# Optimization experiments

Hardware: AMD Instinct MI355X
Metric: run time of the kernel (lower is better)

The kernel has to match this reference:

```python
import jax, jax.numpy as jnp
import numpy as np

B, C, H, W = 4, 256, 64, 64
DQ = C // 8

def setup_inputs() -> dict:
    key = jax.random.key(0)
    ks = jax.random.split(key, 7)
    x = jax.random.normal(ks[0], (B, C, H, W), dtype=jnp.float32)
    # 1x1 convs == per-pixel linear layers: weight [out, in], bias [out]
    Wq = jax.random.normal(ks[1], (DQ, C), dtype=jnp.float32) * (1.0 / np.sqrt(C))
    bq = jax.random.normal(ks[2], (DQ,), dtype=jnp.float32) * 0.01
    Wk = jax.random.normal(ks[3], (DQ, C), dtype=jnp.float32) * (1.0 / np.sqrt(C))
    bk = jax.random.normal(ks[4], (DQ,), dtype=jnp.float32) * 0.01
    Wv = jax.random.normal(ks[5], (C, C), dtype=jnp.float32) * (1.0 / np.sqrt(C))
    bv = jax.random.normal(ks[6], (C,), dtype=jnp.float32) * 0.01
    return {"x": x, "Wq": Wq, "bq": bq, "Wk": Wk, "bk": bk, "Wv": Wv, "bv": bv}

def reference(x, Wq, bq, Wk, bk, Wv, bv):
    b, c, h, w = x.shape
    n = h * w
    xf = x.reshape(b, c, n)                                  # [b,c,n]
    Q = jnp.einsum('dc,bcn->bnd', Wq, xf) + bq               # [b,n,dq]
    K = jnp.einsum('dc,bcn->bdn', Wk, xf) + bk[None, :, None]  # [b,dq,n]
    A = jax.nn.softmax(jnp.einsum('bnd,bdm->bnm', Q, K), axis=-1)  # [b,n,n]
    V = jnp.einsum('oc,bcn->bon', Wv, xf) + bv[None, :, None]      # [b,c,n]
    # torch: bmm(V, A^T) -> out[b,c,i] = sum_j V[b,c,j] * A[b,i,j]
    out = jnp.einsum('bcj,bij->bci', V, A)
    return x + out.reshape(b, c, h, w)
```

## Files before the change

kernel.cpp:

```cpp
#include <hip/hip_runtime.h>
#include <math.h>

#define BB 4
#define CC 256
#define NN 4096
#define DQ 32
#define LOG2E 1.44269504f

typedef _Float16 half8 __attribute__((ext_vector_type(8)));
typedef _Float16 half4 __attribute__((ext_vector_type(4)));
typedef float float4v __attribute__((ext_vector_type(4)));

__global__ __launch_bounds__(64) void prep_kernel(
    const float* __restrict__ Wq, const float* __restrict__ bq,
    const float* __restrict__ Wk, const float* __restrict__ bk,
    const float* __restrict__ Wv, const float* __restrict__ bv,
    _Float16* __restrict__ Wh, float* __restrict__ bh)
{
    int o = blockIdx.x, t = threadIdx.x;
    const float* src; float scale = 1.0f, bias;
    if (o < DQ)            { src = Wq + o * CC;        scale = LOG2E; bias = bq[o] * LOG2E; }
    else if (o < 2 * DQ)   { src = Wk + (o - DQ) * CC;                bias = bk[o - DQ]; }
    else                   { src = Wv + (o - 2 * DQ) * CC;            bias = bv[o - 2 * DQ]; }
    float4 v = *(const float4*)(src + t * 4);
    half4 h = { (_Float16)(v.x * scale), (_Float16)(v.y * scale),
                (_Float16)(v.z * scale), (_Float16)(v.w * scale) };
    *(half4*)(Wh + o * CC + t * 4) = h;
    if (t == 0) bh[o] = bias;
}

__global__ __launch_bounds__(256) void proj_kernel(
    const float* __restrict__ x, const _Float16* __restrict__ Wh,
    const float* __restrict__ bh,
    _Float16* __restrict__ Qt, _Float16* __restrict__ Kt,
    _Float16* __restrict__ Vh)
{
    __shared__ _Float16 xl[32 * 256];
    __shared__ _Float16 os_qk[32 * 72];
    __shared__ _Float16 os_v[256 * 40];

    const int tid = threadIdx.x;
    const int lane = tid & 63, w = tid >> 6;
    const int i16 = lane & 15, q = lane >> 4;
    const int n0 = blockIdx.x * 32, b = blockIdx.y;

    const float* xb = x + (size_t)b * CC * NN + n0;
    #pragma unroll
    for (int u = 0; u < 8; ++u) {
        int idx = u * 256 + tid;
        int c = idx >> 3, n4 = idx & 7;
        float4 v = *(const float4*)(xb + (size_t)c * NN + n4 * 4);
        int chunk = c >> 3, cl = c & 7;
        float vv[4] = {v.x, v.y, v.z, v.w};
        #pragma unroll
        for (int e = 0; e < 4; ++e) {
            int n = n4 * 4 + e;
            xl[n * 256 + ((chunk ^ n) * 8) + cl] = (_Float16)vv[e];
        }
    }

    float4v acc[5][2];
    const int obase = 80 * w;
    #pragma unroll
    for (int ot = 0; ot < 5; ++ot) {
        float4 b4 = *(const float4*)(bh + obase + 16 * ot + 4 * q);
        #pragma unroll
        for (int nt = 0; nt < 2; ++nt)
            acc[ot][nt] = (float4v){b4.x, b4.y, b4.z, b4.w};
    }
    __syncthreads();

    #pragma unroll
    for (int k = 0; k < 8; ++k) {
        half8 af[5], bf[2];
        #pragma unroll
        for (int ot = 0; ot < 5; ++ot)
            af[ot] = *(const half8*)(Wh + (size_t)(obase + 16 * ot + i16) * CC + k * 32 + 8 * q);
        #pragma unroll
        for (int nt = 0; nt < 2; ++nt) {
            int n = 16 * nt + i16;
            bf[nt] = *(const half8*)&xl[n * 256 + (((4 * k + q) ^ n) * 8)];
        }
        #pragma unroll
        for (int ot = 0; ot < 5; ++ot)
            #pragma unroll
            for (int nt = 0; nt < 2; ++nt)
                acc[ot][nt] = __builtin_amdgcn_mfma_f32_16x16x32_f16(af[ot], bf[nt], acc[ot][nt], 0, 0, 0);
    }

    #pragma unroll
    for (int ot = 0; ot < 5; ++ot) {
        int og = obase + 16 * ot;
        #pragma unroll
        for (int nt = 0; nt < 2; ++nt) {
            int n = 16 * nt + i16;
            if (og < 64) {
                half4 hv = { (_Float16)acc[ot][nt][0], (_Float16)acc[ot][nt][1],
                             (_Float16)acc[ot][nt][2], (_Float16)acc[ot][nt][3] };
                *(half4*)&os_qk[n * 72 + og + 4 * q] = hv;
            } else {
                int cb = og - 64 + 4 * q;
                #pragma unroll
                for (int r = 0; r < 4; ++r)
                    os_v[(cb + r) * 40 + n] = (_Float16)acc[ot][nt][r];
            }
        }
    }
    __syncthreads();

    _Float16* Qtb = Qt + (size_t)b * NN * DQ;
    _Float16* Ktb = Kt + (size_t)b * NN * DQ;
    {
        int n = tid >> 3, p = tid & 7;
        half8 hv = *(const half8*)&os_qk[n * 72 + 8 * p];
        if (p < 4) *(half8*)(Qtb + (size_t)(n0 + n) * DQ + 8 * p) = hv;
        else       *(half8*)(Ktb + (size_t)(n0 + n) * DQ + 8 * (p - 4)) = hv;
    }
    _Float16* Vb = Vh + (size_t)b * CC * NN;
    #pragma unroll
    for (int u = 0; u < 4; ++u) {
        int c = u * 64 + (tid >> 2), p = tid & 3;
        half8 hv = *(const half8*)&os_v[c * 40 + 8 * p];
        *(half8*)(Vb + (size_t)c * NN + n0 + 8 * p) = hv;
    }
}

__global__ __launch_bounds__(256) void rowstat_kernel(
    const _Float16* __restrict__ Qt, const _Float16* __restrict__ Kt,
    float* __restrict__ M2, float* __restrict__ L)
{
    const int tid = threadIdx.x;
    const int lane = tid & 63, w = tid >> 6;
    const int i16 = lane & 15, q = lane >> 4;
    const int q0 = blockIdx.x * 64, js = blockIdx.y, b = blockIdx.z;

    const _Float16* Qtb = Qt + (size_t)b * NN * DQ;
    const _Float16* kb  = Kt + (size_t)b * NN * DQ + (size_t)(js * 1024) * DQ;
    half8 qb = *(const half8*)(Qtb + (size_t)(q0 + 16 * w + i16) * DQ + 8 * q);

    half8 ka[4];
    #pragma unroll
    for (int u = 0; u < 4; ++u)
        ka[u] = *(const half8*)(kb + (size_t)(16 * u + i16) * DQ + 8 * q);

    float m = -INFINITY, l = 0.f;
    for (int t = 0; t < 64; t += 4) {
        #pragma unroll
        for (int u = 0; u < 4; ++u) {
            float4v z = {0.f, 0.f, 0.f, 0.f};
            float4v s = __builtin_amdgcn_mfma_f32_16x16x32_f16(ka[u], qb, z, 0, 0, 0);
            int nt = t + 4 + u;
            if (nt < 64)
                ka[u] = *(const half8*)(kb + (size_t)(16 * nt + i16) * DQ + 8 * q);
            m = fmaxf(m, fmaxf(fmaxf(s[0], s[1]), fmaxf(s[2], s[3])));
            l += (exp2f(s[0]) + exp2f(s[1])) + (exp2f(s[2]) + exp2f(s[3]));
        }
    }
    l += __shfl_xor(l, 16, 64);
    l += __shfl_xor(l, 32, 64);
    m = fmaxf(m, __shfl_xor(m, 16, 64));
    m = fmaxf(m, __shfl_xor(m, 32, 64));
    if (q == 0) {
        int qi = q0 + 16 * w + i16;
        M2[((size_t)b * 4 + js) * NN + qi] = m;
        L[((size_t)b * 4 + js) * NN + qi] = l;
    }
}

__global__ __launch_bounds__(256) void attn_kernel(
    const float* __restrict__ x,
    const _Float16* __restrict__ Qt, const _Float16* __restrict__ Kt,
    const _Float16* __restrict__ Vh,
    const float* __restrict__ M2, const float* __restrict__ L,
    float* __restrict__ out)
{
    __shared__ _Float16 k_lds[2][64 * 32];
    __shared__ _Float16 v_lds[3][128 * 64];
    __shared__ _Float16 ps[2][64 * 72];

    const int tid = threadIdx.x;
    const int w = tid >> 6, lane = tid & 63;
    const int i16 = lane & 15, q = lane >> 4;
    const int i0 = blockIdx.x * 64, cs = blockIdx.y, b = blockIdx.z;
    const int c0 = cs * 128;

    const _Float16* Ktb = Kt + (size_t)b * NN * DQ;
    const _Float16* Vb  = Vh + (size_t)b * CC * NN + (size_t)c0 * NN;

    float m2v[4], linv[4];
    #pragma unroll
    for (int it = 0; it < 4; ++it) {
        int qi = i0 + 16 * it + i16;
        float mm = -INFINITY, ll = 0.f;
        #pragma unroll
        for (int p = 0; p < 4; ++p) {
            mm = fmaxf(mm, M2[((size_t)b * 4 + p) * NN + qi]);
            ll += L[((size_t)b * 4 + p) * NN + qi];
        }
        m2v[it] = mm;
        linv[it] = exp2f(mm) / ll;
    }

    half8 qb[4];
    {
        const _Float16* Qtb = Qt + (size_t)b * NN * DQ;
        #pragma unroll
        for (int it = 0; it < 4; ++it)
            qb[it] = *(const half8*)(Qtb + (size_t)(i0 + 16 * it + i16) * DQ + 8 * q);
    }

    float4v O[2][4];
    #pragma unroll
    for (int ct = 0; ct < 2; ++ct)
        #pragma unroll
        for (int it = 0; it < 4; ++it)
            O[ct][it] = (float4v){0.f, 0.f, 0.f, 0.f};

    const int jK = tid >> 2, dgK = tid & 3;
    const int cbV = tid >> 3, jgV = tid & 7;
    const int kaddr = jK * 32 + ((dgK ^ (jK & 3)) * 8);
    int vaddr[4];
    #pragma unroll
    for (int u = 0; u < 4; ++u) {
        int c = u * 32 + cbV;
        vaddr[u] = c * 64 + ((jgV ^ (c & 7)) * 8);
    }

    half8 kv, vv[4];
    kv = *(const half8*)(Ktb + (size_t)jK * DQ + 8 * dgK);
    #pragma unroll
    for (int u = 0; u < 4; ++u)
        vv[u] = *(const half8*)(Vb + (size_t)(u * 32 + cbV) * NN + 8 * jgV);
    *(half8*)&k_lds[0][kaddr] = kv;
    #pragma unroll
    for (int u = 0; u < 4; ++u)
        *(half8*)&v_lds[0][vaddr[u]] = vv[u];
    kv = *(const half8*)(Ktb + (size_t)(64 + jK) * DQ + 8 * dgK);
    #pragma unroll
    for (int u = 0; u < 4; ++u)
        vv[u] = *(const half8*)(Vb + (size_t)(u * 32 + cbV) * NN + 64 + 8 * jgV);

    for (int t = 0; t <= 64; ++t) {
        __syncthreads();
        if (t < 63) {
            *(half8*)&k_lds[(t + 1) & 1][kaddr] = kv;
            const int vn = (t + 1) % 3;
            #pragma unroll
            for (int u = 0; u < 4; ++u)
                *(half8*)&v_lds[vn][vaddr[u]] = vv[u];
        }
        if (t < 62) {
            int jn = (t + 2) * 64;
            kv = *(const half8*)(Ktb + (size_t)(jn + jK) * DQ + 8 * dgK);
            #pragma unroll
            for (int u = 0; u < 4; ++u)
                vv[u] = *(const half8*)(Vb + (size_t)(u * 32 + cbV) * NN + jn + 8 * jgV);
        }
        if (t > 0) {
            const _Float16* psp = ps[(t - 1) & 1];
            const _Float16* vp  = v_lds[(t - 1) % 3];
            half8 pb[2][4];
            #pragma unroll
            for (int ks = 0; ks < 2; ++ks)
                #pragma unroll
                for (int it = 0; it < 4; ++it)
                    pb[ks][it] = *(const half8*)&psp[(16 * it + i16) * 72 + 32 * ks + 8 * q];
            __builtin_amdgcn_s_setprio(1);
            #pragma unroll
            for (int ct = 0; ct < 2; ++ct) {
                int c = 32 * w + 16 * ct + i16;
                #pragma unroll
                for (int ks = 0; ks < 2; ++ks) {
                    int g = 4 * ks + q;
                    half8 va = *(const half8*)&vp[c * 64 + ((g ^ (c & 7)) * 8)];
                    #pragma unroll
                    for (int it = 0; it < 4; ++it)
                        O[ct][it] = __builtin_amdgcn_mfma_f32_16x16x32_f16(va, pb[ks][it], O[ct][it], 0, 0, 0);
                }
            }
            __builtin_amdgcn_s_setprio(0);
        }
        if (t < 64) {
            int j = 16 * w + i16;
            half8 ka = *(const half8*)&k_lds[t & 1][j * 32 + ((q ^ (j & 3)) * 8)];
            _Float16* psc = ps[t & 1];
            #pragma unroll
            for (int it = 0; it < 4; ++it) {
                float4v z = {0.f, 0.f, 0.f, 0.f};
                float4v s = __builtin_amdgcn_mfma_f32_16x16x32_f16(ka, qb[it], z, 0, 0, 0);
                half4 hv = { (_Float16)exp2f(s[0] - m2v[it]),
                             (_Float16)exp2f(s[1] - m2v[it]),
                             (_Float16)exp2f(s[2] - m2v[it]),
                             (_Float16)exp2f(s[3] - m2v[it]) };
                *(half4*)&psc[(16 * it + i16) * 72 + 16 * w + 4 * q] = hv;
            }
        }
    }

    const float* xb = x + (size_t)b * CC * NN;
    float* ob = out + (size_t)b * CC * NN;
    #pragma unroll
    for (int ct = 0; ct < 2; ++ct)
        #pragma unroll
        for (int it = 0; it < 4; ++it)
            #pragma unroll
            for (int r = 0; r < 4; ++r) {
                int c = c0 + 32 * w + 16 * ct + 4 * q + r;
                size_t idx = (size_t)c * NN + i0 + 16 * it + i16;
                ob[idx] = xb[idx] + O[ct][it][r] * linv[it];
            }
}

extern "C" void kernel_launch(void* const* d_in, const int* in_sizes, int n_in,
                              void* d_out, int out_size, void* d_ws, size_t ws_size,
                              hipStream_t stream) {
    const float* x  = (const float*)d_in[0];
    const float* Wq = (const float*)d_in[1];
    const float* bq = (const float*)d_in[2];
    const float* Wk = (const float*)d_in[3];
    const float* bk = (const float*)d_in[4];
    const float* Wv = (const float*)d_in[5];
    const float* bv = (const float*)d_in[6];
    float* out = (float*)d_out;

    char* ws = (char*)d_ws;
    _Float16* Wh = (_Float16*)(ws);
    float*    bh = (float*)(ws + 163840);
    _Float16* Qt = (_Float16*)(ws + 262144);
    _Float16* Kt = (_Float16*)(ws + 1310720);
    _Float16* Vh = (_Float16*)(ws + 2359296);
    float*    M2 = (float*)(ws + 10747904);
    float*    L  = (float*)(ws + 11010048);

    prep_kernel<<<dim3(320), 64, 0, stream>>>(Wq, bq, Wk, bk, Wv, bv, Wh, bh);
    proj_kernel<<<dim3(NN / 32, BB), 256, 0, stream>>>(x, Wh, bh, Qt, Kt, Vh);
    rowstat_kernel<<<dim3(NN / 64, 4, BB), 256, 0, stream>>>(Qt, Kt, M2, L);
    attn_kernel<<<dim3(NN / 64, 2, BB), 256, 0, stream>>>(x, Qt, Kt, Vh, M2, L, out);
}
```

Baseline: 196.3 us.

## Fuse row-statistics pass into attention kernel and drop separate launch

Removes the standalone rowstat kernel and computes per-row softmax max and sum inside the attention kernel. The four waves each scan a quarter of the keys and combine their results via shared memory. This removes a kernel launch and the global write/read of the M2/L buffers. In exchange, each of the two channel-split blocks recomputes the same statistics, doubling the QK and exp work for that pass.

```diff
diff --git a/kernel.cpp b/kernel.cpp
--- a/kernel.cpp
+++ b/kernel.cpp
@@ -125,58 +125,17 @@
     }
 }
 
-__global__ __launch_bounds__(256) void rowstat_kernel(
-    const _Float16* __restrict__ Qt, const _Float16* __restrict__ Kt,
-    float* __restrict__ M2, float* __restrict__ L)
-{
-    const int tid = threadIdx.x;
-    const int lane = tid & 63, w = tid >> 6;
-    const int i16 = lane & 15, q = lane >> 4;
-    const int q0 = blockIdx.x * 64, js = blockIdx.y, b = blockIdx.z;
-
-    const _Float16* Qtb = Qt + (size_t)b * NN * DQ;
-    const _Float16* kb  = Kt + (size_t)b * NN * DQ + (size_t)(js * 1024) * DQ;
-    half8 qb = *(const half8*)(Qtb + (size_t)(q0 + 16 * w + i16) * DQ + 8 * q);
-
-    half8 ka[4];
-    #pragma unroll
-    for (int u = 0; u < 4; ++u)
-        ka[u] = *(const half8*)(kb + (size_t)(16 * u + i16) * DQ + 8 * q);
-
-    float m = -INFINITY, l = 0.f;
-    for (int t = 0; t < 64; t += 4) {
-        #pragma unroll
-        for (int u = 0; u < 4; ++u) {
-            float4v z = {0.f, 0.f, 0.f, 0.f};
-            float4v s = __builtin_amdgcn_mfma_f32_16x16x32_f16(ka[u], qb, z, 0, 0, 0);
-            int nt = t + 4 + u;
-            if (nt < 64)
-                ka[u] = *(const half8*)(kb + (size_t)(16 * nt + i16) * DQ + 8 * q);
-            m = fmaxf(m, fmaxf(fmaxf(s[0], s[1]), fmaxf(s[2], s[3])));
-            l += (exp2f(s[0]) + exp2f(s[1])) + (exp2f(s[2]) + exp2f(s[3]));
-        }
-    }
-    l += __shfl_xor(l, 16, 64);
-    l += __shfl_xor(l, 32, 64);
-    m = fmaxf(m, __shfl_xor(m, 16, 64));
-    m = fmaxf(m, __shfl_xor(m, 32, 64));
-    if (q == 0) {
-        int qi = q0 + 16 * w + i16;
-        M2[((size_t)b * 4 + js) * NN + qi] = m;
-        L[((size_t)b * 4 + js) * NN + qi] = l;
-    }
-}
-
 __global__ __launch_bounds__(256) void attn_kernel(
     const float* __restrict__ x,
     const _Float16* __restrict__ Qt, const _Float16* __restrict__ Kt,
     const _Float16* __restrict__ Vh,
-    const float* __restrict__ M2, const float* __restrict__ L,
     float* __restrict__ out)
 {
     __shared__ _Float16 k_lds[2][64 * 32];
     __shared__ _Float16 v_lds[3][128 * 64];
     __shared__ _Float16 ps[2][64 * 72];
+    __shared__ float    st_m[4][64];
+    __shared__ float    st_l[4][64];
 
     const int tid = threadIdx.x;
     const int w = tid >> 6, lane = tid & 63;
@@ -187,26 +146,72 @@
     const _Float16* Ktb = Kt + (size_t)b * NN * DQ;
     const _Float16* Vb  = Vh + (size_t)b * CC * NN + (size_t)c0 * NN;
 
-    float m2v[4], linv[4];
-    #pragma unroll
-    for (int it = 0; it < 4; ++it) {
-        int qi = i0 + 16 * it + i16;
-        float mm = -INFINITY, ll = 0.f;
-        #pragma unroll
-        for (int p = 0; p < 4; ++p) {
-            mm = fmaxf(mm, M2[((size_t)b * 4 + p) * NN + qi]);
-            ll += L[((size_t)b * 4 + p) * NN + qi];
-        }
-        m2v[it] = mm;
-        linv[it] = exp2f(mm) / ll;
-    }
-
     half8 qb[4];
     {
         const _Float16* Qtb = Qt + (size_t)b * NN * DQ;
         #pragma unroll
         for (int it = 0; it < 4; ++it)
             qb[it] = *(const half8*)(Qtb + (size_t)(i0 + 16 * it + i16) * DQ + 8 * q);
+    }
+
+    float mA[4] = {-INFINITY, -INFINITY, -INFINITY, -INFINITY};
+    float lA[4] = {0.f, 0.f, 0.f, 0.f};
+    {
+        const _Float16* kq = Ktb + (size_t)(1024 * w) * DQ;
+        half8 kfr0 = *(const half8*)(kq + (size_t)i16 * DQ + 8 * q);
+        half8 kfr1 = *(const half8*)(kq + (size_t)(16 + i16) * DQ + 8 * q);
+        for (int t = 0; t < 64; t += 2) {
+            {
+                half8 ka = kfr0;
+                if (t + 2 < 64)
+                    kfr0 = *(const half8*)(kq + (size_t)(16 * (t + 2) + i16) * DQ + 8 * q);
+                #pragma unroll
+                for (int it = 0; it < 4; ++it) {
+                    float4v z = {0.f, 0.f, 0.f, 0.f};
+                    float4v s = __builtin_amdgcn_mfma_f32_16x16x32_f16(ka, qb[it], z, 0, 0, 0);
+                    mA[it] = fmaxf(mA[it], fmaxf(fmaxf(s[0], s[1]), fmaxf(s[2], s[3])));
+                    lA[it] += (exp2f(s[0]) + exp2f(s[1])) + (exp2f(s[2]) + exp2f(s[3]));
+                }
+            }
+            {
+                half8 ka = kfr1;
+                if (t + 3 < 64)
+                    kfr1 = *(const half8*)(kq + (size_t)(16 * (t + 3) + i16) * DQ + 8 * q);
+                #pragma unroll
+                for (int it = 0; it < 4; ++it) {
+                    float4v z = {0.f, 0.f, 0.f, 0.f};
+                    float4v s = __builtin_amdgcn_mfma_f32_16x16x32_f16(ka, qb[it], z, 0, 0, 0);
+                    mA[it] = fmaxf(mA[it], fmaxf(fmaxf(s[0], s[1]), fmaxf(s[2], s[3])));
+                    lA[it] += (exp2f(s[0]) + exp2f(s[1])) + (exp2f(s[2]) + exp2f(s[3]));
+                }
+            }
+        }
+        #pragma unroll
+        for (int it = 0; it < 4; ++it) {
+            lA[it] += __shfl_xor(lA[it], 16, 64);
+            lA[it] += __shfl_xor(lA[it], 32, 64);
+            mA[it] = fmaxf(mA[it], __shfl_xor(mA[it], 16, 64));
+            mA[it] = fmaxf(mA[it], __shfl_xor(mA[it], 32, 64));
+        }
+        if (q == 0) {
+            #pragma unroll
+            for (int it = 0; it < 4; ++it) {
+                st_m[w][16 * it + i16] = mA[it];
+                st_l[w][16 * it + i16] = lA[it];
+            }
+        }
+    }
+    __syncthreads();
+
+    float m2v[4], linv[4];
+    #pragma unroll
+    for (int it = 0; it < 4; ++it) {
+        int qrow = 16 * it + i16;
+        float mm = fmaxf(fmaxf(st_m[0][qrow], st_m[1][qrow]),
+                         fmaxf(st_m[2][qrow], st_m[3][qrow]));
+        float ll = (st_l[0][qrow] + st_l[1][qrow]) + (st_l[2][qrow] + st_l[3][qrow]);
+        m2v[it] = mm;
+        linv[it] = exp2f(mm) / ll;
     }
 
     float4v O[2][4];
@@ -329,11 +334,8 @@
     _Float16* Qt = (_Float16*)(ws + 262144);
     _Float16* Kt = (_Float16*)(ws + 1310720);
     _Float16* Vh = (_Float16*)(ws + 2359296);
-    float*    M2 = (float*)(ws + 10747904);
-    float*    L  = (float*)(ws + 11010048);
 
     prep_kernel<<<dim3(320), 64, 0, stream>>>(Wq, bq, Wk, bk, Wv, bv, Wh, bh);
     proj_kernel<<<dim3(NN / 32, BB), 256, 0, stream>>>(x, Wh, bh, Qt, Kt, Vh);
-    rowstat_kernel<<<dim3(NN / 64, 4, BB), 256, 0, stream>>>(Qt, Kt, M2, L);
-    attn_kernel<<<dim3(NN / 64, 2, BB), 256, 0, stream>>>(x, Qt, Kt, Vh, M2, L, out);
+    attn_kernel<<<dim3(NN / 64, 2, BB), 256, 0, stream>>>(x, Qt, Kt, Vh, out);
 }
```

Result: slower. 214.4 us (+9.2%).
